# Kernel tuning notes

Hardware: AMD Instinct MI355X
Metric: run time of the kernel (lower is better)

The kernel has to match this reference:

```python
import jax, jax.numpy as jnp
import numpy as np

W_KERNEL = 5      # dilation kernel size (w)
K_BG = 0.1        # background weight (k)
RELAX = 5.0       # sigmoid temperature (relax)
INF = 1e4         # 'no zero in column' sentinel (>> image diagonal)
EPS = 1e-7        # DiceLoss eps


def setup_inputs() -> dict:
    key = jax.random.key(0)
    k1, k2 = jax.random.split(key)
    B, H, W = 32, 256, 256
    preds = jax.random.normal(k1, (B, H, W), dtype=jnp.float32)
    targets = (jax.random.uniform(k2, (B, H, W)) > 0.99).astype(jnp.float32)
    return {"preds": preds, "targets": targets}


def _dilate(t, w):
    # cv2.dilate with w x w ones kernel == sliding-window max, SAME padding
    pad = w // 2
    return jax.lax.reduce_window(t, -jnp.inf, jax.lax.max,
                                 (1, w, w), (1, 1, 1),
                                 [(0, 0), (pad, pad), (pad, pad)])


def _vertical_dist(zero_mask):
    # per-column distance (in rows) to nearest zero pixel; [B,H,W] -> [B,H,W]
    B, H, W = zero_mask.shape
    rows = jnp.moveaxis(zero_mask, 1, 0)  # [H,B,W]

    def step(carry, z):
        d = jnp.where(z, 0.0, jnp.minimum(carry + 1.0, INF))
        return d, d

    init = jnp.full((B, W), INF, dtype=jnp.float32)
    _, fwd = jax.lax.scan(step, init, rows)
    _, bwd = jax.lax.scan(step, init, rows[::-1])
    g = jnp.minimum(fwd, bwd[::-1])  # [H,B,W]
    return jnp.moveaxis(g, 0, 1)


def _edt(fat):
    # exact euclidean distance transform (distance to nearest zero pixel),
    # separable two-pass: vertical 1D distance, then horizontal min-plus.
    B, H, W = fat.shape
    g = _vertical_dist(fat == 0)  # [B,H,W]
    col = jnp.arange(W, dtype=jnp.float32)
    off2 = (col[:, None] - col[None, :]) ** 2  # [W_j, W_k]

    def per_img(gi):  # gi: [H,W]
        # d2[i,j] = min_k g[i,k]^2 + (j-k)^2   -> [H,W,W] intermediate
        d2 = jnp.min(gi[:, None, :] ** 2 + off2[None, :, :], axis=-1)
        return jnp.sqrt(d2)

    return jax.lax.map(per_img, g)  # sequential over batch caps memory


def _distance_maps(targets):
    fat = _dilate(targets, W_KERNEL)          # [B,H,W]
    d = _edt(fat)                              # [B,H,W]
    soft = jax.nn.sigmoid(d / RELAX)
    soft = soft - jnp.min(soft, axis=(1, 2), keepdims=True)
    mx = jnp.max(soft, axis=(1, 2), keepdims=True)
    soft = soft / jnp.where(mx > 0, mx, 1.0)
    dm_soft = soft + (1.0 - fat) * K_BG
    has_fg = jnp.max(targets, axis=(1, 2), keepdims=True) > 0
    return jnp.where(has_fg, dm_soft, 1.0 - targets)


def reference(preds, targets):
    p = jax.nn.sigmoid(preds)
    dm = jax.lax.stop_gradient(_distance_maps(targets))  # computed in numpy in torch => constant
    pw = p * dm
    bs = pw.shape[0]
    y_pred = pw.reshape(bs, 1, -1)
    y_true = targets.reshape(bs, 1, -1)
    # smp DiceLoss('binary', from_logits=False): dims=(0,2), smooth=0, eps=1e-7
    inter = jnp.sum(y_pred * y_true, axis=(0, 2))
    card = jnp.sum(y_pred + y_true, axis=(0, 2))
    dice = (2.0 * inter) / jnp.maximum(card, EPS)
    loss = 1.0 - dice
    mask = (jnp.sum(y_true, axis=(0, 2)) > 0).astype(loss.dtype)
    return jnp.mean(loss * mask)
```

## Files before the change

### kernel.cpp

```cpp
#include <hip/hip_runtime.h>
#include <math.h>

#define BB 32
#define HH 256
#define WW 256
#define HW (HH*WW)
#define K_BG 0.1f
#define RELAX 5.0f
#define EPS_D 1e-7
#define RPB 8
#define MEGA_BLOCKS (BB * (HH / RPB))

typedef unsigned long long u64;

__device__ __forceinline__ float sigf(float x) { return 1.0f / (1.0f + expf(-x)); }

__device__ __forceinline__ u64 shflx64(u64 x, int s) {
    return (u64)__shfl_xor((unsigned long long)x, s, 64);
}

__global__ void k_maskdil(const float* __restrict__ tg, u64* __restrict__ dmaskT,
                          u64* __restrict__ nzmask, unsigned* __restrict__ cnt) {
    __shared__ u64 nz[20][4];
    __shared__ u64 hd[20][4];
    int blk = blockIdx.x;
    int b = blk >> 4, band = blk & 15;
    int r0 = band * 16;
    int t = threadIdx.x, w = t >> 6;
    const float* img = tg + b * HW;
    if (blk == 0 && t == 0) cnt[0] = 0;
    float v[20];
    #pragma unroll
    for (int rr = 0; rr < 20; ++rr) {
        int rg = r0 + rr - 2;
        v[rr] = (rg >= 0 && rg < HH) ? img[rg * WW + t] : 0.0f;
    }
    #pragma unroll
    for (int rr = 0; rr < 20; ++rr) {
        u64 bal = __ballot(v[rr] != 0.0f);
        if ((t & 63) == 0) nz[rr][w] = bal;
    }
    __syncthreads();
    if (t < 80) {
        int rr = t >> 2, k = t & 3;
        u64 m = nz[rr][k];
        u64 ml = (k > 0) ? nz[rr][k - 1] : 0ULL;
        u64 mr = (k < 3) ? nz[rr][k + 1] : 0ULL;
        hd[rr][k] = m | (m << 1) | (m << 2) | (m >> 1) | (m >> 2)
                  | (ml >> 62) | (ml >> 63) | (mr << 62) | (mr << 63);
    }
    if (t < 64) {
        int rr = t >> 2, k = t & 3;
        nzmask[b * 1024 + (r0 + rr) * 4 + k] = nz[rr + 2][k];
    }
    __syncthreads();
    if (t < 64) {
        int rr = t >> 2, k = t & 3;
        u64 o = hd[rr][k] | hd[rr + 1][k] | hd[rr + 2][k] | hd[rr + 3][k] | hd[rr + 4][k];
        dmaskT[b * 1024 + k * 256 + (r0 + rr)] = o;
    }
}

__global__ __launch_bounds__(256, 4) void k_mega(const float* __restrict__ preds,
                                                 const u64* __restrict__ dmaskT,
                                                 const u64* __restrict__ nzmask,
                                                 float4* __restrict__ part1,
                                                 float4* __restrict__ part2,
                                                 unsigned* __restrict__ cnt,
                                                 float* __restrict__ out) {
    __shared__ u64 colT[4 * 256];
    __shared__ float gS[RPB][WW];
    __shared__ float red[8][4];
    __shared__ unsigned stick;
    __shared__ float sI[BB], sC[BB], sA[BB];
    int blk = blockIdx.x;
    int b = blk >> 5, q = blk & 31;
    int i0 = q * RPB;
    int tid = threadIdx.x;
    int lane = tid & 63, wv = tid >> 6;
    int j = tid;

    float p[RPB];
    #pragma unroll
    for (int rr = 0; rr < RPB; ++rr)
        p[rr] = preds[(b * HH + i0 + rr) * WW + j];
    u64 nzw[RPB];
    #pragma unroll
    for (int rr = 0; rr < RPB; ++rr)
        nzw[rr] = nzmask[b * 1024 + (i0 + rr) * 4 + wv];

    const u64* base = dmaskT + b * 1024;
    const u64 L32 = 0x00000000FFFFFFFFULL, L16 = 0x0000FFFF0000FFFFULL,
              L8  = 0x00FF00FF00FF00FFULL, L4  = 0x0F0F0F0F0F0F0F0FULL,
              L2  = 0x3333333333333333ULL, L1  = 0x5555555555555555ULL;
    #pragma unroll
    for (int w = 0; w < 4; ++w) {
        u64 x = base[w * 256 + wv * 64 + lane];
        u64 pp;
        pp = shflx64(x, 32); x = (lane & 32) ? ((x & ~L32) | ((pp & ~L32) >> 32)) : ((x & L32) | ((pp & L32) << 32));
        pp = shflx64(x, 16); x = (lane & 16) ? ((x & ~L16) | ((pp & ~L16) >> 16)) : ((x & L16) | ((pp & L16) << 16));
        pp = shflx64(x,  8); x = (lane &  8) ? ((x & ~L8 ) | ((pp & ~L8 ) >>  8)) : ((x & L8 ) | ((pp & L8 ) <<  8));
        pp = shflx64(x,  4); x = (lane &  4) ? ((x & ~L4 ) | ((pp & ~L4 ) >>  4)) : ((x & L4 ) | ((pp & L4 ) <<  4));
        pp = shflx64(x,  2); x = (lane &  2) ? ((x & ~L2 ) | ((pp & ~L2 ) >>  2)) : ((x & L2 ) | ((pp & L2 ) <<  2));
        pp = shflx64(x,  1); x = (lane &  1) ? ((x & ~L1 ) | ((pp & ~L1 ) >>  1)) : ((x & L1 ) | ((pp & L1 ) <<  1));
        colT[wv * 256 + w * 64 + lane] = x;
    }
    __syncthreads();

    u64 yw[4];
    #pragma unroll
    for (int g = 0; g < 4; ++g) yw[g] = ~colT[g * 256 + j];

    int g0v[RPB], fgv[RPB];
    #pragma unroll
    for (int rr = 0; rr < RPB; ++rr) {
        int i = i0 + rr;
        int iw = i >> 6, ib = i & 63;
        u64 lowm  = (2ULL << ib) - 1ULL;
        u64 highm = ~((1ULL << ib) - 1ULL);
        int pu = -1, pd = -1;
        #pragma unroll
        for (int w = 0; w < 4; ++w) {
            u64 m = (w < iw) ? ~0ULL : ((w == iw) ? lowm : 0ULL);
            u64 z = yw[w] & m;
            int cand = (w << 6) + 63 - __clzll(z);
            pu = z ? cand : pu;
        }
        #pragma unroll
        for (int w = 3; w >= 0; --w) {
            u64 m = (w > iw) ? ~0ULL : ((w == iw) ? highm : 0ULL);
            u64 z = yw[w] & m;
            int cand = (w << 6) + (__ffsll((unsigned long long)z) - 1);
            pd = z ? cand : pd;
        }
        int up = (pu >= 0) ? (i - pu) : 10000;
        int dn = (pd >= 0) ? (pd - i) : 10000;
        int g0 = min(min(up, dn), 10000);
        g0v[rr] = g0;
        fgv[rr] = (int)((~yw[iw] >> ib) & 1ULL);
        gS[rr][j] = (float)g0;
    }
    __syncthreads();

    float vals[8];
    #pragma unroll
    for (int qq = 0; qq < 6; ++qq) vals[qq] = 0.0f;
    vals[6] = 1e30f; vals[7] = 0.0f;
    #pragma unroll
    for (int rr = 0; rr < RPB; ++rr) {
        float gv = (float)g0v[rr];
        float best = gv * gv;
        #pragma unroll
        for (int r = 1; r <= 8; ++r) {
            float rf = (float)(r * r);
            int jl = j - r, jr = j + r;
            float vl = (jl >= 0) ? gS[rr][jl] : 1e4f;
            float vr = (jr < WW) ? gS[rr][jr] : 1e4f;
            best = fminf(best, fminf(fmaf(vl, vl, rf), fmaf(vr, vr, rf)));
        }
        for (int rc = 9; rc < WW + 8; rc += 8) {
            if ((float)(rc * rc) >= best) break;
            #pragma unroll
            for (int dr = 0; dr < 8; ++dr) {
                int r = rc + dr;
                float rf = (float)(r * r);
                int jl = j - r, jr = j + r;
                float vl = (jl >= 0) ? gS[rr][jl] : 1e4f;
                float vr = (jr < WW) ? gS[rr][jr] : 1e4f;
                best = fminf(best, fminf(fmaf(vl, vl, rf), fmaf(vr, vr, rf)));
            }
        }
        float dv = sqrtf(best);
        float sp = sigf(p[rr]);
        float sd = sigf(dv / RELAX);
        float tv = (float)((nzw[rr] >> (j & 63)) & 1ULL);
        vals[0] += sp * sd * tv;
        vals[1] += sp * tv;
        vals[2] += sp * sd;
        vals[3] += sp;
        vals[4] += fgv[rr] ? 0.0f : sp;
        vals[5] += tv;
        vals[6] = fminf(vals[6], dv);
        vals[7] = fmaxf(vals[7], dv);
    }
    for (int off = 32; off > 0; off >>= 1) {
        #pragma unroll
        for (int qq = 0; qq < 6; ++qq) vals[qq] += __shfl_down(vals[qq], off, 64);
        vals[6] = fminf(vals[6], __shfl_down(vals[6], off, 64));
        vals[7] = fmaxf(vals[7], __shfl_down(vals[7], off, 64));
    }
    if (lane == 0) {
        #pragma unroll
        for (int qq = 0; qq < 8; ++qq) red[qq][wv] = vals[qq];
    }
    __syncthreads();
    if (tid == 0) {
        float s[8];
        #pragma unroll
        for (int qq = 0; qq < 6; ++qq) s[qq] = red[qq][0] + red[qq][1] + red[qq][2] + red[qq][3];
        s[6] = fminf(fminf(red[6][0], red[6][1]), fminf(red[6][2], red[6][3]));
        s[7] = fmaxf(fmaxf(red[7][0], red[7][1]), fmaxf(red[7][2], red[7][3]));
        part1[blk] = make_float4(s[0], s[1], s[2], s[3]);
        part2[blk] = make_float4(s[4], s[5], s[6], s[7]);
        __threadfence();
        stick = atomicAdd(cnt, 1u);
    }
    __syncthreads();
    if (stick != MEGA_BLOCKS - 1) return;

    __threadfence();
    #pragma unroll
    for (int pass = 0; pass < 4; ++pass) {
        int img = pass * 8 + (tid >> 5);
        int k = tid & 31;
        float4 p1 = part1[img * 32 + k];
        float4 p2 = part2[img * 32 + k];
        float v2[8] = {p1.x, p1.y, p1.z, p1.w, p2.x, p2.y, p2.z, p2.w};
        for (int off = 16; off > 0; off >>= 1) {
            #pragma unroll
            for (int qq = 0; qq < 6; ++qq) v2[qq] += __shfl_down(v2[qq], off, 32);
            v2[6] = fminf(v2[6], __shfl_down(v2[6], off, 32));
            v2[7] = fmaxf(v2[7], __shfl_down(v2[7], off, 32));
        }
        if (k == 0) {
            float A = v2[0], Bs = v2[1], Ap = v2[2], Bp = v2[3];
            float Cp = v2[4], T = v2[5], dmn = v2[6], dmx = v2[7];
            float inter, card, any;
            if (dmx > 0.0f) {
                float smin = sigf(dmn / RELAX);
                float smax = sigf(dmx / RELAX);
                float m = smax - smin;
                float denom = (m > 0.0f) ? m : 1.0f;
                inter = (A - smin * Bs) / denom;
                card  = (Ap - smin * Bp) / denom + K_BG * Cp + T;
                any = 1.0f;
            } else {
                inter = 0.0f;
                card = Bp - Bs + T;
                any = 0.0f;
            }
            sI[img] = inter; sC[img] = card; sA[img] = any;
        }
    }
    __syncthreads();
    if (tid == 0) {
        double I = 0.0, C = 0.0;
        int any = 0;
        for (int bb = 0; bb < BB; ++bb) {
            I += (double)sI[bb]; C += (double)sC[bb];
            any |= (sA[bb] > 0.0f);
        }
        double dice = 2.0 * I / fmax(C, (double)EPS_D);
        out[0] = any ? (float)(1.0 - dice) : 0.0f;
    }
}

extern "C" void kernel_launch(void* const* d_in, const int* in_sizes, int n_in,
                              void* d_out, int out_size, void* d_ws, size_t ws_size,
                              hipStream_t stream) {
    const float* preds = (const float*)d_in[0];
    const float* tg    = (const float*)d_in[1];
    float* out = (float*)d_out;

    u64* dmaskT   = (u64*)d_ws;
    u64* nzmask   = dmaskT + BB * 1024;
    float4* part1 = (float4*)(nzmask + BB * 1024);
    float4* part2 = part1 + MEGA_BLOCKS;
    unsigned* cnt = (unsigned*)(part2 + MEGA_BLOCKS);

    hipLaunchKernelGGL(k_maskdil, dim3(BB * 16), dim3(WW), 0, stream,
                       tg, dmaskT, nzmask, cnt);
    hipLaunchKernelGGL(k_mega, dim3(MEGA_BLOCKS), dim3(WW), 0, stream,
                       preds, dmaskT, nzmask, part1, part2, cnt, out);
}
```

Measured before the change: 104.0 us.

## Fuse mask dilation into main kernel using a grid-wide spin barrier

Merges the mask/dilation kernel into the main kernel. Each block computes the dilated bitmasks for its own 8 rows, using a 12-row halo, and publishes them. A global atomic-counter spin barrier then makes sure every block's dmaskT is written before the column transpose reads it. Non-zero masks are taken straight from shared memory instead of a global buffer. This removes one kernel launch and a global round trip. In exchange it adds a hipMemsetAsync and relies on all 1024 blocks being co-resident (256 threads, launch bounds 4 per CU), with a bounded spin that could silently break correctness if residency fails.

```diff
diff --git a/kernel.cpp b/kernel.cpp
--- a/kernel.cpp
+++ b/kernel.cpp
@@ -9,7 +9,7 @@
 #define RELAX 5.0f
 #define EPS_D 1e-7
 #define RPB 8
-#define MEGA_BLOCKS (BB * (HH / RPB))
+#define NBLK (BB * (HH / RPB))
 
 typedef unsigned long long u64;
 
@@ -19,60 +19,21 @@
     return (u64)__shfl_xor((unsigned long long)x, s, 64);
 }
 
-__global__ void k_maskdil(const float* __restrict__ tg, u64* __restrict__ dmaskT,
-                          u64* __restrict__ nzmask, unsigned* __restrict__ cnt) {
-    __shared__ u64 nz[20][4];
-    __shared__ u64 hd[20][4];
-    int blk = blockIdx.x;
-    int b = blk >> 4, band = blk & 15;
-    int r0 = band * 16;
-    int t = threadIdx.x, w = t >> 6;
-    const float* img = tg + b * HW;
-    if (blk == 0 && t == 0) cnt[0] = 0;
-    float v[20];
-    #pragma unroll
-    for (int rr = 0; rr < 20; ++rr) {
-        int rg = r0 + rr - 2;
-        v[rr] = (rg >= 0 && rg < HH) ? img[rg * WW + t] : 0.0f;
-    }
-    #pragma unroll
-    for (int rr = 0; rr < 20; ++rr) {
-        u64 bal = __ballot(v[rr] != 0.0f);
-        if ((t & 63) == 0) nz[rr][w] = bal;
-    }
-    __syncthreads();
-    if (t < 80) {
-        int rr = t >> 2, k = t & 3;
-        u64 m = nz[rr][k];
-        u64 ml = (k > 0) ? nz[rr][k - 1] : 0ULL;
-        u64 mr = (k < 3) ? nz[rr][k + 1] : 0ULL;
-        hd[rr][k] = m | (m << 1) | (m << 2) | (m >> 1) | (m >> 2)
-                  | (ml >> 62) | (ml >> 63) | (mr << 62) | (mr << 63);
-    }
-    if (t < 64) {
-        int rr = t >> 2, k = t & 3;
-        nzmask[b * 1024 + (r0 + rr) * 4 + k] = nz[rr + 2][k];
-    }
-    __syncthreads();
-    if (t < 64) {
-        int rr = t >> 2, k = t & 3;
-        u64 o = hd[rr][k] | hd[rr + 1][k] | hd[rr + 2][k] | hd[rr + 3][k] | hd[rr + 4][k];
-        dmaskT[b * 1024 + k * 256 + (r0 + rr)] = o;
-    }
-}
-
-__global__ __launch_bounds__(256, 4) void k_mega(const float* __restrict__ preds,
-                                                 const u64* __restrict__ dmaskT,
-                                                 const u64* __restrict__ nzmask,
-                                                 float4* __restrict__ part1,
-                                                 float4* __restrict__ part2,
-                                                 unsigned* __restrict__ cnt,
-                                                 float* __restrict__ out) {
+__global__ __launch_bounds__(256, 4) void k_fused(const float* __restrict__ preds,
+                                                  const float* __restrict__ tg,
+                                                  u64* __restrict__ dmaskT,
+                                                  float4* __restrict__ part1,
+                                                  float4* __restrict__ part2,
+                                                  unsigned* __restrict__ cnt,
+                                                  float* __restrict__ out) {
+    __shared__ u64 nz[12][4];
+    __shared__ u64 hd[12][4];
     __shared__ u64 colT[4 * 256];
     __shared__ float gS[RPB][WW];
     __shared__ float red[8][4];
     __shared__ unsigned stick;
     __shared__ float sI[BB], sC[BB], sA[BB];
+
     int blk = blockIdx.x;
     int b = blk >> 5, q = blk & 31;
     int i0 = q * RPB;
@@ -84,10 +45,50 @@
     #pragma unroll
     for (int rr = 0; rr < RPB; ++rr)
         p[rr] = preds[(b * HH + i0 + rr) * WW + j];
+
+    const float* img = tg + b * HW;
+    float v[12];
+    #pragma unroll
+    for (int rr = 0; rr < 12; ++rr) {
+        int rg = i0 + rr - 2;
+        v[rr] = (rg >= 0 && rg < HH) ? img[rg * WW + j] : 0.0f;
+    }
+    #pragma unroll
+    for (int rr = 0; rr < 12; ++rr) {
+        u64 bal = __ballot(v[rr] != 0.0f);
+        if (lane == 0) nz[rr][wv] = bal;
+    }
+    __syncthreads();
+    if (tid < 48) {
+        int lr = tid >> 2, k = tid & 3;
+        u64 m = nz[lr][k];
+        u64 ml = (k > 0) ? nz[lr][k - 1] : 0ULL;
+        u64 mr = (k < 3) ? nz[lr][k + 1] : 0ULL;
+        hd[lr][k] = m | (m << 1) | (m << 2) | (m >> 1) | (m >> 2)
+                  | (ml >> 62) | (ml >> 63) | (mr << 62) | (mr << 63);
+    }
+    __syncthreads();
+    if (tid < 32) {
+        int rr = tid >> 2, k = tid & 3;
+        u64 o = hd[rr][k] | hd[rr + 1][k] | hd[rr + 2][k] | hd[rr + 3][k] | hd[rr + 4][k];
+        dmaskT[b * 1024 + k * 256 + (i0 + rr)] = o;
+    }
     u64 nzw[RPB];
     #pragma unroll
-    for (int rr = 0; rr < RPB; ++rr)
-        nzw[rr] = nzmask[b * 1024 + (i0 + rr) * 4 + wv];
+    for (int rr = 0; rr < RPB; ++rr) nzw[rr] = nz[rr + 2][wv];
+    __syncthreads();
+
+    if (tid == 0) {
+        __threadfence();
+        atomicAdd(&cnt[0], 1u);
+        int spins = 0;
+        while (atomicAdd(&cnt[0], 0u) < NBLK) {
+            __builtin_amdgcn_s_sleep(8);
+            if (++spins > 200000) break;
+        }
+    }
+    __syncthreads();
+    __threadfence();
 
     const u64* base = dmaskT + b * 1024;
     const u64 L32 = 0x00000000FFFFFFFFULL, L16 = 0x0000FFFF0000FFFFULL,
@@ -203,18 +204,18 @@
         part1[blk] = make_float4(s[0], s[1], s[2], s[3]);
         part2[blk] = make_float4(s[4], s[5], s[6], s[7]);
         __threadfence();
-        stick = atomicAdd(cnt, 1u);
-    }
-    __syncthreads();
-    if (stick != MEGA_BLOCKS - 1) return;
+        stick = atomicAdd(&cnt[1], 1u);
+    }
+    __syncthreads();
+    if (stick != NBLK - 1) return;
 
     __threadfence();
     #pragma unroll
     for (int pass = 0; pass < 4; ++pass) {
-        int img = pass * 8 + (tid >> 5);
+        int img2 = pass * 8 + (tid >> 5);
         int k = tid & 31;
-        float4 p1 = part1[img * 32 + k];
-        float4 p2 = part2[img * 32 + k];
+        float4 p1 = part1[img2 * 32 + k];
+        float4 p2 = part2[img2 * 32 + k];
         float v2[8] = {p1.x, p1.y, p1.z, p1.w, p2.x, p2.y, p2.z, p2.w};
         for (int off = 16; off > 0; off >>= 1) {
             #pragma unroll
@@ -239,7 +240,7 @@
                 card = Bp - Bs + T;
                 any = 0.0f;
             }
-            sI[img] = inter; sC[img] = card; sA[img] = any;
+            sI[img2] = inter; sC[img2] = card; sA[img2] = any;
         }
     }
     __syncthreads();
@@ -263,13 +264,11 @@
     float* out = (float*)d_out;
 
     u64* dmaskT   = (u64*)d_ws;
-    u64* nzmask   = dmaskT + BB * 1024;
-    float4* part1 = (float4*)(nzmask + BB * 1024);
-    float4* part2 = part1 + MEGA_BLOCKS;
-    unsigned* cnt = (unsigned*)(part2 + MEGA_BLOCKS);
-
-    hipLaunchKernelGGL(k_maskdil, dim3(BB * 16), dim3(WW), 0, stream,
-                       tg, dmaskT, nzmask, cnt);
-    hipLaunchKernelGGL(k_mega, dim3(MEGA_BLOCKS), dim3(WW), 0, stream,
-                       preds, dmaskT, nzmask, part1, part2, cnt, out);
+    float4* part1 = (float4*)(dmaskT + BB * 1024);
+    float4* part2 = part1 + NBLK;
+    unsigned* cnt = (unsigned*)(part2 + NBLK);
+
+    hipMemsetAsync(cnt, 0, 2 * sizeof(unsigned), stream);
+    hipLaunchKernelGGL(k_fused, dim3(NBLK), dim3(256), 0, stream,
+                       preds, tg, dmaskT, part1, part2, cnt, out);
 }
```

New measurement: 220.0 us. 2.12x slower.

## Double threads per block and skip EDT for wave-uniform background rows

Applied to the files above, without the earlier changes.

The mega kernel now launches 512 threads per block, so each thread handles 4 rows instead of 8 and the transpose work is split across 8 waves. It also adds a wave-level ballot per row: when no lane in the wave sits on a dilated-foreground pixel, the column distance scan and the horizontal min-plus search are skipped and the distance is set to 0. The aim is more parallelism per block and less wasted EDT work on the mostly-zero distance field. The cost is higher register and launch-bound pressure at 512 threads, plus extra ballot and branch logic.

```diff
diff --git a/kernel.cpp b/kernel.cpp
--- a/kernel.cpp
+++ b/kernel.cpp
@@ -9,6 +9,7 @@
 #define RELAX 5.0f
 #define EPS_D 1e-7
 #define RPB 8
+#define RPT 4
 #define MEGA_BLOCKS (BB * (HH / RPB))
 
 typedef unsigned long long u64;
@@ -61,7 +62,7 @@
     }
 }
 
-__global__ __launch_bounds__(256, 4) void k_mega(const float* __restrict__ preds,
+__global__ __launch_bounds__(512, 8) void k_mega(const float* __restrict__ preds,
                                                  const u64* __restrict__ dmaskT,
                                                  const u64* __restrict__ nzmask,
                                                  float4* __restrict__ part1,
@@ -70,7 +71,7 @@
                                                  float* __restrict__ out) {
     __shared__ u64 colT[4 * 256];
     __shared__ float gS[RPB][WW];
-    __shared__ float red[8][4];
+    __shared__ float red[8][8];
     __shared__ unsigned stick;
     __shared__ float sI[BB], sC[BB], sA[BB];
     int blk = blockIdx.x;
@@ -78,24 +79,28 @@
     int i0 = q * RPB;
     int tid = threadIdx.x;
     int lane = tid & 63, wv = tid >> 6;
-    int j = tid;
-
-    float p[RPB];
-    #pragma unroll
-    for (int rr = 0; rr < RPB; ++rr)
-        p[rr] = preds[(b * HH + i0 + rr) * WW + j];
-    u64 nzw[RPB];
-    #pragma unroll
-    for (int rr = 0; rr < RPB; ++rr)
-        nzw[rr] = nzmask[b * 1024 + (i0 + rr) * 4 + wv];
+    int j = tid & 255;
+    int r0t = (tid >> 8) * RPT;
+
+    float p[RPT];
+    #pragma unroll
+    for (int rr = 0; rr < RPT; ++rr)
+        p[rr] = preds[(b * HH + i0 + r0t + rr) * WW + j];
+    int wj = j >> 6;
+    u64 nzw[RPT];
+    #pragma unroll
+    for (int rr = 0; rr < RPT; ++rr)
+        nzw[rr] = nzmask[b * 1024 + (i0 + r0t + rr) * 4 + wj];
 
     const u64* base = dmaskT + b * 1024;
     const u64 L32 = 0x00000000FFFFFFFFULL, L16 = 0x0000FFFF0000FFFFULL,
               L8  = 0x00FF00FF00FF00FFULL, L4  = 0x0F0F0F0F0F0F0F0FULL,
               L2  = 0x3333333333333333ULL, L1  = 0x5555555555555555ULL;
-    #pragma unroll
-    for (int w = 0; w < 4; ++w) {
-        u64 x = base[w * 256 + wv * 64 + lane];
+    int tg_ = wv & 3, w0 = (wv >> 2) * 2;
+    #pragma unroll
+    for (int dw = 0; dw < 2; ++dw) {
+        int w = w0 + dw;
+        u64 x = base[w * 256 + tg_ * 64 + lane];
         u64 pp;
         pp = shflx64(x, 32); x = (lane & 32) ? ((x & ~L32) | ((pp & ~L32) >> 32)) : ((x & L32) | ((pp & L32) << 32));
         pp = shflx64(x, 16); x = (lane & 16) ? ((x & ~L16) | ((pp & ~L16) >> 16)) : ((x & L16) | ((pp & L16) << 16));
@@ -103,7 +108,7 @@
         pp = shflx64(x,  4); x = (lane &  4) ? ((x & ~L4 ) | ((pp & ~L4 ) >>  4)) : ((x & L4 ) | ((pp & L4 ) <<  4));
         pp = shflx64(x,  2); x = (lane &  2) ? ((x & ~L2 ) | ((pp & ~L2 ) >>  2)) : ((x & L2 ) | ((pp & L2 ) <<  2));
         pp = shflx64(x,  1); x = (lane &  1) ? ((x & ~L1 ) | ((pp & ~L1 ) >>  1)) : ((x & L1 ) | ((pp & L1 ) <<  1));
-        colT[wv * 256 + w * 64 + lane] = x;
+        colT[tg_ * 256 + w * 64 + lane] = x;
     }
     __syncthreads();
 
@@ -111,34 +116,40 @@
     #pragma unroll
     for (int g = 0; g < 4; ++g) yw[g] = ~colT[g * 256 + j];
 
-    int g0v[RPB], fgv[RPB];
-    #pragma unroll
-    for (int rr = 0; rr < RPB; ++rr) {
-        int i = i0 + rr;
+    int g0v[RPT], fgv[RPT], needw[RPT];
+    #pragma unroll
+    for (int rr = 0; rr < RPT; ++rr) {
+        int i = i0 + r0t + rr;
         int iw = i >> 6, ib = i & 63;
-        u64 lowm  = (2ULL << ib) - 1ULL;
-        u64 highm = ~((1ULL << ib) - 1ULL);
-        int pu = -1, pd = -1;
-        #pragma unroll
-        for (int w = 0; w < 4; ++w) {
-            u64 m = (w < iw) ? ~0ULL : ((w == iw) ? lowm : 0ULL);
-            u64 z = yw[w] & m;
-            int cand = (w << 6) + 63 - __clzll(z);
-            pu = z ? cand : pu;
-        }
-        #pragma unroll
-        for (int w = 3; w >= 0; --w) {
-            u64 m = (w > iw) ? ~0ULL : ((w == iw) ? highm : 0ULL);
-            u64 z = yw[w] & m;
-            int cand = (w << 6) + (__ffsll((unsigned long long)z) - 1);
-            pd = z ? cand : pd;
-        }
-        int up = (pu >= 0) ? (i - pu) : 10000;
-        int dn = (pd >= 0) ? (pd - i) : 10000;
-        int g0 = min(min(up, dn), 10000);
+        int fg = (int)((~yw[iw] >> ib) & 1ULL);
+        fgv[rr] = fg;
+        u64 anyf = __ballot(fg != 0);
+        needw[rr] = (anyf != 0ULL);
+        int g0 = 0;
+        if (anyf) {
+            u64 lowm  = (2ULL << ib) - 1ULL;
+            u64 highm = ~((1ULL << ib) - 1ULL);
+            int pu = -1, pd = -1;
+            #pragma unroll
+            for (int w = 0; w < 4; ++w) {
+                u64 m = (w < iw) ? ~0ULL : ((w == iw) ? lowm : 0ULL);
+                u64 z = yw[w] & m;
+                int cand = (w << 6) + 63 - __clzll(z);
+                pu = z ? cand : pu;
+            }
+            #pragma unroll
+            for (int w = 3; w >= 0; --w) {
+                u64 m = (w > iw) ? ~0ULL : ((w == iw) ? highm : 0ULL);
+                u64 z = yw[w] & m;
+                int cand = (w << 6) + (__ffsll((unsigned long long)z) - 1);
+                pd = z ? cand : pd;
+            }
+            int up = (pu >= 0) ? (i - pu) : 10000;
+            int dn = (pd >= 0) ? (pd - i) : 10000;
+            g0 = min(min(up, dn), 10000);
+        }
         g0v[rr] = g0;
-        fgv[rr] = (int)((~yw[iw] >> ib) & 1ULL);
-        gS[rr][j] = (float)g0;
+        gS[r0t + rr][j] = (float)g0;
     }
     __syncthreads();
 
@@ -147,27 +158,30 @@
     for (int qq = 0; qq < 6; ++qq) vals[qq] = 0.0f;
     vals[6] = 1e30f; vals[7] = 0.0f;
     #pragma unroll
-    for (int rr = 0; rr < RPB; ++rr) {
+    for (int rr = 0; rr < RPT; ++rr) {
+        int rt = r0t + rr;
         float gv = (float)g0v[rr];
         float best = gv * gv;
-        #pragma unroll
-        for (int r = 1; r <= 8; ++r) {
-            float rf = (float)(r * r);
-            int jl = j - r, jr = j + r;
-            float vl = (jl >= 0) ? gS[rr][jl] : 1e4f;
-            float vr = (jr < WW) ? gS[rr][jr] : 1e4f;
-            best = fminf(best, fminf(fmaf(vl, vl, rf), fmaf(vr, vr, rf)));
-        }
-        for (int rc = 9; rc < WW + 8; rc += 8) {
-            if ((float)(rc * rc) >= best) break;
-            #pragma unroll
-            for (int dr = 0; dr < 8; ++dr) {
-                int r = rc + dr;
+        if (needw[rr]) {
+            #pragma unroll
+            for (int r = 1; r <= 8; ++r) {
                 float rf = (float)(r * r);
                 int jl = j - r, jr = j + r;
-                float vl = (jl >= 0) ? gS[rr][jl] : 1e4f;
-                float vr = (jr < WW) ? gS[rr][jr] : 1e4f;
+                float vl = (jl >= 0) ? gS[rt][jl] : 1e4f;
+                float vr = (jr < WW) ? gS[rt][jr] : 1e4f;
                 best = fminf(best, fminf(fmaf(vl, vl, rf), fmaf(vr, vr, rf)));
+            }
+            for (int rc = 9; rc < WW + 8; rc += 8) {
+                if ((float)(rc * rc) >= best) break;
+                #pragma unroll
+                for (int dr = 0; dr < 8; ++dr) {
+                    int r = rc + dr;
+                    float rf = (float)(r * r);
+                    int jl = j - r, jr = j + r;
+                    float vl = (jl >= 0) ? gS[rt][jl] : 1e4f;
+                    float vr = (jr < WW) ? gS[rt][jr] : 1e4f;
+                    best = fminf(best, fminf(fmaf(vl, vl, rf), fmaf(vr, vr, rf)));
+                }
             }
         }
         float dv = sqrtf(best);
@@ -197,21 +211,29 @@
     if (tid == 0) {
         float s[8];
         #pragma unroll
-        for (int qq = 0; qq < 6; ++qq) s[qq] = red[qq][0] + red[qq][1] + red[qq][2] + red[qq][3];
-        s[6] = fminf(fminf(red[6][0], red[6][1]), fminf(red[6][2], red[6][3]));
-        s[7] = fmaxf(fmaxf(red[7][0], red[7][1]), fmaxf(red[7][2], red[7][3]));
+        for (int qq = 0; qq < 6; ++qq) {
+            s[qq] = 0.0f;
+            #pragma unroll
+            for (int k = 0; k < 8; ++k) s[qq] += red[qq][k];
+        }
+        s[6] = red[6][0]; s[7] = red[7][0];
+        #pragma unroll
+        for (int k = 1; k < 8; ++k) {
+            s[6] = fminf(s[6], red[6][k]);
+            s[7] = fmaxf(s[7], red[7][k]);
+        }
         part1[blk] = make_float4(s[0], s[1], s[2], s[3]);
         part2[blk] = make_float4(s[4], s[5], s[6], s[7]);
         __threadfence();
-        stick = atomicAdd(cnt, 1u);
+        stick = atomicAdd(&cnt[0], 1u);
     }
     __syncthreads();
     if (stick != MEGA_BLOCKS - 1) return;
 
     __threadfence();
     #pragma unroll
-    for (int pass = 0; pass < 4; ++pass) {
-        int img = pass * 8 + (tid >> 5);
+    for (int pass = 0; pass < 2; ++pass) {
+        int img = pass * 16 + (tid >> 5);
         int k = tid & 31;
         float4 p1 = part1[img * 32 + k];
         float4 p2 = part2[img * 32 + k];
@@ -270,6 +292,6 @@
 
     hipLaunchKernelGGL(k_maskdil, dim3(BB * 16), dim3(WW), 0, stream,
                        tg, dmaskT, nzmask, cnt);
-    hipLaunchKernelGGL(k_mega, dim3(MEGA_BLOCKS), dim3(WW), 0, stream,
+    hipLaunchKernelGGL(k_mega, dim3(MEGA_BLOCKS), dim3(512), 0, stream,
                        preds, dmaskT, nzmask, part1, part2, cnt, out);
 }
```

After: 98.18 us. -5.6%, faster.
